# Performance work log

Hardware: AMD Instinct MI355X
Metric: run time of the kernel (lower is better)

Reference implementation:

```python
import jax, jax.numpy as jnp
import numpy as np

B, N, NODE_DIM = 64, 64, 192
H = 256          # node_hidden_dim
PDIM = 64        # property_embedding_dim
NUM_EDGE_TYPE = 5
T = 4            # message-passing rounds
E = 16384        # total edges (flattened batched graph)
E_SEL = 65536    # selected candidate pairs


def setup_inputs() -> dict:
    key = jax.random.key(0)
    ks = jax.random.split(key, 24)
    def g(k, shape, scale=0.05):
        return jax.random.normal(k, shape, dtype=jnp.float32) * scale
    inp = {
        "x": jax.random.normal(ks[0], (B, N, NODE_DIM), dtype=jnp.float32),
        "edge_index": jax.random.randint(ks[1], (2, E), 0, B * N, dtype=jnp.int32),
        "edge_attr": jax.random.uniform(ks[2], (E, NUM_EDGE_TYPE), dtype=jnp.float32),
        "props": jax.random.normal(ks[3], (B, 1), dtype=jnp.float32),
        "sel_b": jax.random.randint(ks[4], (E_SEL,), 0, B, dtype=jnp.int32),
        "sel_i": jax.random.randint(ks[5], (E_SEL,), 0, N, dtype=jnp.int32),
        "sel_j": jax.random.randint(ks[6], (E_SEL,), 0, N, dtype=jnp.int32),
        "golden_edge": jax.random.randint(ks[7], (E_SEL,), 0, NUM_EDGE_TYPE, dtype=jnp.int32),
        # parameters
        "W_prop": g(ks[8], (1, PDIM)), "b_prop": jnp.zeros((PDIM,), jnp.float32),
        "W_in": g(ks[9], (NODE_DIM, H)), "b_in": jnp.zeros((H,), jnp.float32),
        "W_msg": g(ks[10], (H + NUM_EDGE_TYPE, H)), "b_msg": jnp.zeros((H,), jnp.float32),
        "W_upd": g(ks[11], (2 * H, H)), "b_upd": jnp.zeros((H,), jnp.float32),
        "W_add": g(ks[12], (H + PDIM, H)), "b_add": jnp.zeros((H,), jnp.float32),
        "W1": g(ks[13], (2 * H, H)), "b1": jnp.zeros((H,), jnp.float32),
        "W2": g(ks[14], (H, H)), "b2": jnp.zeros((H,), jnp.float32),
        "W3": g(ks[15], (H, 2 * H)), "b3": jnp.zeros((2 * H,), jnp.float32),
        "W_out": g(ks[16], (2 * H, NUM_EDGE_TYPE)), "b_out": jnp.zeros((NUM_EDGE_TYPE,), jnp.float32),
    }
    return inp


def reference(x, edge_index, edge_attr, props, sel_b, sel_i, sel_j, golden_edge,
              W_prop, b_prop, W_in, b_in, W_msg, b_msg, W_upd, b_upd,
              W_add, b_add, W1, b1, W2, b2, W3, b3, W_out, b_out):
    BN = B * N
    node_x = x.reshape(BN, NODE_DIM)
    src, dst = edge_index[0], edge_index[1]

    # --- GNN node embedding (t rounds of message passing, opaque Encoder.embed_node) ---
    h = jax.nn.relu(node_x @ W_in + b_in)                       # [BN, H]
    for _ in range(T):
        msg_in = jnp.concatenate([h[src], edge_attr], axis=-1)  # [E, H+num_edge_type]
        msg = jax.nn.relu(msg_in @ W_msg + b_msg)               # [E, H]
        agg = jax.ops.segment_sum(msg, dst, num_segments=BN)    # [BN, H]
        h = jax.nn.relu(jnp.concatenate([h, agg], axis=-1) @ W_upd + b_upd)

    node_emb = h.reshape(B, N, H)

    # --- property conditioning + addition linear ---
    prop = props @ W_prop + b_prop                               # [B, PDIM]
    propp = jnp.broadcast_to(prop[:, None, :], (B, N, PDIM))
    node_embg = jnp.concatenate([node_emb, propp], axis=-1) @ W_add + b_add  # [B, N, H]

    # --- gather selected (src, dst) pairs directly (equiv. to repeat_interleave + boolean mask) ---
    flat = node_embg.reshape(BN, H)
    src_e = flat[sel_b * N + sel_i]                              # [E_SEL, H]
    dst_e = flat[sel_b * N + sel_j]                              # [E_SEL, H]
    pair = jnp.concatenate([src_e, dst_e], axis=-1)              # [E_SEL, 2H]

    # --- edge predictor MLP (3 layers, ReLU between) + output linear ---
    h1 = jax.nn.relu(pair @ W1 + b1)
    h2 = jax.nn.relu(h1 @ W2 + b2)
    h3 = h2 @ W3 + b3
    logits = h3 @ W_out + b_out                                  # [E_SEL, num_edge_type]

    # --- cross entropy (mean) ---
    logp = jax.nn.log_softmax(logits, axis=-1)
    loss = -jnp.mean(jnp.take_along_axis(logp, golden_edge[:, None].astype(jnp.int32), axis=-1))
    return loss
```

## Files before the change

kernel.cpp:

```cpp
#include <hip/hip_runtime.h>
#include <math.h>

#define BN 4096
#define N_PER_B 64
#define NE 16384
#define NSEL 65536
#define NET 5
#define PD 64
#define H1STR 260
#define FSTR 264

typedef float f32x4 __attribute__((ext_vector_type(4)));
typedef float f32x16 __attribute__((ext_vector_type(16)));
typedef short short8 __attribute__((ext_vector_type(8)));
typedef short short4v __attribute__((ext_vector_type(4)));

__device__ __forceinline__ unsigned short f2bf(float f) {
    unsigned int u = __builtin_bit_cast(unsigned int, f);
    u += 0x7fff + ((u >> 16) & 1);
    return (unsigned short)(u >> 16);
}
__device__ __forceinline__ float bf_lo(unsigned int u) {
    return __builtin_bit_cast(float, u << 16);
}
__device__ __forceinline__ float bf_hi(unsigned int u) {
    return __builtin_bit_cast(float, u & 0xffff0000u);
}
__device__ __forceinline__ unsigned int pack2(float a, float b) {
    return (unsigned)f2bf(a) | ((unsigned)f2bf(b) << 16);
}
__device__ __forceinline__ short8 ld_frag(const unsigned short* p) {
    const short4v lo = *(const short4v*)(p);
    const short4v hi = *(const short4v*)(p + 4);
    return __builtin_shufflevector(lo, hi, 0, 1, 2, 3, 4, 5, 6, 7);
}
__device__ __forceinline__ unsigned int addrelu2(unsigned int a, unsigned int b, unsigned int c) {
    const float lo = fmaxf(bf_lo(a) + bf_lo(b) + bf_lo(c), 0.f);
    const float hi = fmaxf(bf_hi(a) + bf_hi(b) + bf_hi(c), 0.f);
    return pack2(lo, hi);
}

__global__ __launch_bounds__(256) void k_hist(const int* __restrict__ eidx,
                                              int* __restrict__ deg)
{
    const int e = blockIdx.x * 256 + threadIdx.x;
    atomicAdd(&deg[eidx[NE + e]], 1);
}

__global__ __launch_bounds__(256) void csr_scan(const int* __restrict__ deg,
                                                int* __restrict__ row_start,
                                                int* __restrict__ cursor)
{
    __shared__ int sums[256];
    const int tid = threadIdx.x;
    const int base = tid * 16;
    int local[16];
    int s = 0;
    #pragma unroll
    for (int i = 0; i < 16; ++i) { local[i] = s; s += deg[base + i]; }
    sums[tid] = s;
    __syncthreads();
    for (int off = 1; off < 256; off <<= 1) {
        const int v = sums[tid];
        const int add = (tid >= off) ? sums[tid - off] : 0;
        __syncthreads();
        sums[tid] = v + add;
        __syncthreads();
    }
    const int offset = (tid == 0) ? 0 : sums[tid - 1];
    #pragma unroll
    for (int i = 0; i < 16; ++i) {
        const int v = offset + local[i];
        row_start[base + i] = v;
        cursor[base + i] = v;
    }
    if (tid == 255) row_start[4096] = NE;
}

__global__ __launch_bounds__(256) void csr_scatter(const int* __restrict__ eidx,
                                                   int* __restrict__ cursor,
                                                   int* __restrict__ srcs,
                                                   int* __restrict__ epos)
{
    const int e = blockIdx.x * 256 + threadIdx.x;
    const int pos = atomicAdd(&cursor[eidx[NE + e]], 1);
    srcs[pos] = eidx[e];
    epos[e] = pos;
}

__global__ __launch_bounds__(256) void k_pre(
    const float* __restrict__ W_in, const float* __restrict__ W_msg,
    const float* __restrict__ W_upd, const float* __restrict__ W_add,
    const float* __restrict__ W1, const float* __restrict__ W2,
    const float* __restrict__ W3, const float* __restrict__ b3,
    const float* __restrict__ W_out, const float* __restrict__ b_out,
    const float* __restrict__ props, const float* __restrict__ W_prop,
    const float* __restrict__ b_prop, const float* __restrict__ b_add,
    const float* __restrict__ b_msg, const float* __restrict__ eattr,
    const int* __restrict__ epos,
    unsigned short* __restrict__ wbf, unsigned short* __restrict__ WfT,
    float* __restrict__ bfv, float* __restrict__ prop_add,
    unsigned short* __restrict__ ETc)
{
    __shared__ __align__(16) char smem[16704];
    const int blk = blockIdx.x;
    const int tid = threadIdx.x;

    if (blk < 128) {
        float (*s)[65] = (float(*)[65])smem;
        const int wsel = blk >> 4;
        const int sub = blk & 15;
        const float* src; unsigned short* dst; int K = 256;
        switch (wsel) {
            case 0: src = W_in;              dst = wbf;                         K = 192; break;
            case 1: src = W_msg;             dst = wbf + 49152;                 break;
            case 2: src = W_upd;             dst = wbf + 49152 + 65536;         break;
            case 3: src = W_upd + 256 * 256; dst = wbf + 49152 + 2 * 65536;     break;
            case 4: src = W_add;             dst = wbf + 49152 + 3 * 65536;     break;
            case 5: src = W1;                dst = wbf + 49152 + 4 * 65536;     break;
            case 6: src = W1 + 256 * 256;    dst = wbf + 49152 + 5 * 65536;     break;
            default: src = W2;               dst = wbf + 49152 + 6 * 65536;     break;
        }
        const int k0 = (sub >> 2) * 64;
        const int n0 = (sub & 3) * 64;
        if (k0 >= K) return;
        const int tn = tid & 63;
        const int tg = tid >> 6;
        #pragma unroll
        for (int i = 0; i < 16; ++i) {
            const int kk = tg * 16 + i;
            s[kk][tn] = src[(size_t)(k0 + kk) * 256 + n0 + tn];
        }
        __syncthreads();
        #pragma unroll
        for (int i = 0; i < 16; ++i) {
            const int nn = tg * 16 + i;
            dst[(size_t)(n0 + nn) * K + k0 + tn] = f2bf(s[tn][nn]);
        }
    } else if (blk < 192) {
        const int b = blk - 128;
        const float pv = props[b];
        float acc = b_add[tid];
        for (int p = 0; p < PD; ++p) {
            const float e = fmaf(pv, W_prop[p], b_prop[p]);
            acc = fmaf(e, W_add[(256 + p) * 256 + tid], acc);
        }
        prop_add[b * 256 + tid] = acc;
    } else if (blk < 449) {
        float* part = (float*)smem;
        const int cb = blk - 192;
        float acc[NET] = {0.f, 0.f, 0.f, 0.f, 0.f};
        #pragma unroll
        for (int rep = 0; rep < 2; ++rep) {
            const int j = rep * 256 + tid;
            const float wv = (cb < 256) ? W3[(size_t)cb * 512 + j] : b3[j];
            #pragma unroll
            for (int t = 0; t < NET; ++t) acc[t] = fmaf(wv, W_out[j * NET + t], acc[t]);
        }
        #pragma unroll
        for (int t = 0; t < NET; ++t)
            for (int off = 32; off >= 1; off >>= 1) acc[t] += __shfl_down(acc[t], off);
        if ((tid & 63) == 0) {
            #pragma unroll
            for (int t = 0; t < NET; ++t) part[(tid >> 6) * NET + t] = acc[t];
        }
        __syncthreads();
        if (tid == 0) {
            float s[NET];
            #pragma unroll
            for (int t = 0; t < NET; ++t)
                s[t] = part[t] + part[NET + t] + part[2 * NET + t] + part[3 * NET + t];
            if (cb < 256) {
                #pragma unroll
                for (int t = 0; t < NET; ++t) WfT[t * 256 + cb] = f2bf(s[t]);
                #pragma unroll
                for (int t = NET; t < 16; ++t) WfT[t * 256 + cb] = 0;
            } else {
                #pragma unroll
                for (int t = 0; t < NET; ++t) bfv[t] = s[t] + b_out[t];
            }
        }
    } else {
        float* ea = (float*)smem;
        int* eposs = (int*)(smem + 2560 + 64);
        const int eb = (blk - 449) * 128;
        if (tid < 160)
            *(float4*)&ea[tid * 4] = *(const float4*)(eattr + (size_t)eb * 5 + tid * 4);
        if (tid < 128) eposs[tid] = epos[eb + tid];
        __syncthreads();
        const float* Wme = W_msg + 256 * 256;
        const float w0 = Wme[0 * 256 + tid];
        const float w1 = Wme[1 * 256 + tid];
        const float w2 = Wme[2 * 256 + tid];
        const float w3 = Wme[3 * 256 + tid];
        const float w4 = Wme[4 * 256 + tid];
        const float bm = b_msg[tid];
        for (int i = 0; i < 128; ++i) {
            const float* a = ea + i * 5;
            float v = bm;
            v = fmaf(a[0], w0, v); v = fmaf(a[1], w1, v); v = fmaf(a[2], w2, v);
            v = fmaf(a[3], w3, v); v = fmaf(a[4], w4, v);
            ETc[(size_t)eposs[i] * 256 + tid] = f2bf(v);
        }
    }
}

__global__ __launch_bounds__(1024) void fstep(
    const float* __restrict__ x, const unsigned short* __restrict__ hbuf,
    const unsigned short* __restrict__ Pin, const unsigned short* __restrict__ ETc,
    const int* __restrict__ row_start, const int* __restrict__ srcs,
    const unsigned short* __restrict__ WaT, const unsigned short* __restrict__ WbT,
    const float* __restrict__ bias1,
    const unsigned short* __restrict__ Wp2T, const float* __restrict__ prop_add,
    const unsigned short* __restrict__ W1aT, const unsigned short* __restrict__ W1bT,
    unsigned short* __restrict__ hout, unsigned short* __restrict__ out1,
    unsigned short* __restrict__ out2, int mode)
{
    __shared__ __align__(16) unsigned short Hg[16 * FSTR];
    __shared__ __align__(16) unsigned short Ag[16 * FSTR];
    __shared__ __align__(16) unsigned short Hs[16 * FSTR];
    __shared__ __align__(16) unsigned short H2s[16 * FSTR];
    const int tid = threadIdx.x;
    const int w = tid >> 6;
    const int lane = tid & 63;
    const int q = lane >> 4;
    const int tx = lane & 15;
    const int m0 = blockIdx.x * 16;
    const int col = w * 16 + tx;

    if (mode != 0) {
        {
            const int r = tid >> 6;
            const int c4 = (tid & 63) * 4;
            *(uint2*)&Hg[r * FSTR + c4] =
                *(const uint2*)(hbuf + (size_t)(m0 + r) * 256 + c4);
        }
        {
            const int node = m0 + w;
            const int beg = row_start[node];
            const int end = row_start[node + 1];
            const int c = lane * 4;
            float a0 = 0.f, a1 = 0.f, a2 = 0.f, a3 = 0.f;
            for (int idx = beg; idx < end; ++idx) {
                const int src = srcs[idx];
                const uint2 pu = *(const uint2*)(Pin + (size_t)src * 256 + c);
                const uint2 eu = *(const uint2*)(ETc + (size_t)idx * 256 + c);
                a0 += fmaxf(bf_lo(pu.x) + bf_lo(eu.x), 0.f);
                a1 += fmaxf(bf_hi(pu.x) + bf_hi(eu.x), 0.f);
                a2 += fmaxf(bf_lo(pu.y) + bf_lo(eu.y), 0.f);
                a3 += fmaxf(bf_hi(pu.y) + bf_hi(eu.y), 0.f);
            }
            uint2 o; o.x = pack2(a0, a1); o.y = pack2(a2, a3);
            *(uint2*)&Ag[w * FSTR + c] = o;
        }
        __syncthreads();
    }

    f32x4 acc = (f32x4)0.f;
    if (mode == 0) {
        #pragma unroll
        for (int s = 0; s < 6; ++s) {
            const int k0 = s * 32;
            const float* ap = x + (size_t)(m0 + tx) * 192 + k0 + q * 8;
            const float4 v0 = *(const float4*)ap;
            const float4 v1 = *(const float4*)(ap + 4);
            short8 af;
            af[0] = (short)f2bf(v0.x); af[1] = (short)f2bf(v0.y);
            af[2] = (short)f2bf(v0.z); af[3] = (short)f2bf(v0.w);
            af[4] = (short)f2bf(v1.x); af[5] = (short)f2bf(v1.y);
            af[6] = (short)f2bf(v1.z); af[7] = (short)f2bf(v1.w);
            const short8 bfr = *(const short8*)(WaT + (size_t)col * 192 + k0 + q * 8);
            acc = __builtin_amdgcn_mfma_f32_16x16x32_bf16(af, bfr, acc, 0, 0, 0);
        }
    } else {
        #pragma unroll
        for (int s = 0; s < 8; ++s) {
            const int k0 = s * 32;
            const short8 af = *(const short8*)&Hg[tx * FSTR + k0 + q * 8];
            const short8 bfr = *(const short8*)(WaT + (size_t)col * 256 + k0 + q * 8);
            acc = __builtin_amdgcn_mfma_f32_16x16x32_bf16(af, bfr, acc, 0, 0, 0);
        }
        #pragma unroll
        for (int s = 0; s < 8; ++s) {
            const int k0 = s * 32;
            const short8 af = *(const short8*)&Ag[tx * FSTR + k0 + q * 8];
            const short8 bfr = *(const short8*)(WbT + (size_t)col * 256 + k0 + q * 8);
            acc = __builtin_amdgcn_mfma_f32_16x16x32_bf16(af, bfr, acc, 0, 0, 0);
        }
    }
    {
        const float bv = bias1[col];
        #pragma unroll
        for (int r = 0; r < 4; ++r) {
            const int row = q * 4 + r;
            const unsigned short us = f2bf(fmaxf(acc[r] + bv, 0.f));
            Hs[row * FSTR + col] = us;
            if (mode < 2) hout[(size_t)(m0 + row) * 256 + col] = us;
        }
    }
    __syncthreads();

    acc = (f32x4)0.f;
    #pragma unroll
    for (int s = 0; s < 8; ++s) {
        const int k0 = s * 32;
        const short8 af = *(const short8*)&Hs[tx * FSTR + k0 + q * 8];
        const short8 bfr = *(const short8*)(Wp2T + (size_t)col * 256 + k0 + q * 8);
        acc = __builtin_amdgcn_mfma_f32_16x16x32_bf16(af, bfr, acc, 0, 0, 0);
    }
    if (mode < 2) {
        #pragma unroll
        for (int r = 0; r < 4; ++r)
            out1[(size_t)(m0 + q * 4 + r) * 256 + col] = f2bf(acc[r]);
        return;
    }
    {
        const float pv = prop_add[(m0 >> 6) * 256 + col];
        #pragma unroll
        for (int r = 0; r < 4; ++r)
            H2s[(q * 4 + r) * FSTR + col] = f2bf(acc[r] + pv);
    }
    __syncthreads();

    for (int which = 0; which < 2; ++which) {
        const unsigned short* WT = which ? W1bT : W1aT;
        unsigned short* op = which ? out2 : out1;
        acc = (f32x4)0.f;
        #pragma unroll
        for (int s = 0; s < 8; ++s) {
            const int k0 = s * 32;
            const short8 af = *(const short8*)&H2s[tx * FSTR + k0 + q * 8];
            const short8 bfr = *(const short8*)(WT + (size_t)col * 256 + k0 + q * 8);
            acc = __builtin_amdgcn_mfma_f32_16x16x32_bf16(af, bfr, acc, 0, 0, 0);
        }
        #pragma unroll
        for (int r = 0; r < 4; ++r)
            op[(size_t)(m0 + q * 4 + r) * 256 + col] = f2bf(acc[r]);
    }
}

__global__ __launch_bounds__(512) void pair_k(
    const unsigned short* __restrict__ A1t, const unsigned short* __restrict__ A2t,
    const float* __restrict__ b1, const unsigned short* __restrict__ W2T,
    const float* __restrict__ b2, const unsigned short* __restrict__ WfT,
    const float* __restrict__ bfv,
    const int* __restrict__ sel_b, const int* __restrict__ sel_i,
    const int* __restrict__ sel_j, const int* __restrict__ golden,
    float* __restrict__ out)
{
    __shared__ __align__(16) unsigned short sbuf[64 * H1STR];
    __shared__ __align__(16) unsigned short b1s[256];
    __shared__ float Lg[64 * 8];
    __shared__ int sidx[64], didx[64], gold[64];

    const int tid = threadIdx.x;
    const int w = tid >> 6;
    const int lane = tid & 63;
    const int q = lane >> 4;
    const int tx = lane & 15;
    const int m = lane & 31;
    const int hh = lane >> 5;
    const int e0 = blockIdx.x * 64;

    if (tid < 64) {
        const int e = e0 + tid;
        const int b = sel_b[e];
        sidx[tid] = b * N_PER_B + sel_i[e];
        didx[tid] = b * N_PER_B + sel_j[e];
        gold[tid] = golden[e];
    }
    if (tid < 256) b1s[tid] = f2bf(b1[tid]);
    __syncthreads();

    {
        const int p = tid >> 3;
        const int chn = tid & 7;
        const unsigned short* r1 = A1t + (size_t)sidx[p] * 256 + chn * 32;
        const unsigned short* r2 = A2t + (size_t)didx[p] * 256 + chn * 32;
        unsigned short* dbase = sbuf + p * H1STR + chn * 32;
        #pragma unroll
        for (int g = 0; g < 4; ++g) {
            const uint4 u1 = *(const uint4*)(r1 + g * 8);
            const uint4 u2 = *(const uint4*)(r2 + g * 8);
            const uint4 ub = *(const uint4*)(b1s + chn * 32 + g * 8);
            uint2 lo2, hi2;
            lo2.x = addrelu2(u1.x, u2.x, ub.x);
            lo2.y = addrelu2(u1.y, u2.y, ub.y);
            hi2.x = addrelu2(u1.z, u2.z, ub.z);
            hi2.y = addrelu2(u1.w, u2.w, ub.w);
            *(uint2*)(dbase + g * 8) = lo2;
            *(uint2*)(dbase + g * 8 + 4) = hi2;
        }
    }
    __syncthreads();

    const int pt = w & 1;
    const int cg = w >> 1;
    f32x16 acc[2];
    acc[0] = (f32x16)0.f; acc[1] = (f32x16)0.f;

    const unsigned short* arow = sbuf + (size_t)(pt * 32 + m) * H1STR + hh * 8;
    const unsigned short* bb0 = W2T + (size_t)(cg * 64 + m) * 256 + hh * 8;
    #pragma unroll 4
    for (int s = 0; s < 16; ++s) {
        const short8 af = ld_frag(arow + s * 16);
        #pragma unroll
        for (int cc = 0; cc < 2; ++cc) {
            const short8 bfr = *(const short8*)(bb0 + (size_t)cc * 32 * 256 + s * 16);
            acc[cc] = __builtin_amdgcn_mfma_f32_32x32x16_bf16(af, bfr, acc[cc], 0, 0, 0);
        }
    }
    __syncthreads();

    #pragma unroll
    for (int cc = 0; cc < 2; ++cc) {
        const int col = cg * 64 + cc * 32 + m;
        const float bv = b2[col];
        #pragma unroll
        for (int reg = 0; reg < 16; ++reg) {
            const int prow = pt * 32 + (reg & 3) + 8 * (reg >> 2) + 4 * hh;
            sbuf[prow * H1STR + col] = f2bf(fmaxf(acc[cc][reg] + bv, 0.f));
        }
    }
    __syncthreads();

    if (w < 4) {
        f32x4 accL = (f32x4)0.f;
        const unsigned short* a2row = sbuf + (size_t)(w * 16 + tx) * H1STR + q * 8;
        const unsigned short* bWf = WfT + (size_t)tx * 256 + q * 8;
        #pragma unroll
        for (int s = 0; s < 8; ++s) {
            const short8 af = ld_frag(a2row + s * 32);
            const short8 bfr = *(const short8*)(bWf + s * 32);
            accL = __builtin_amdgcn_mfma_f32_16x16x32_bf16(af, bfr, accL, 0, 0, 0);
        }
        if (tx < NET) {
            const float bb = bfv[tx];
            #pragma unroll
            for (int reg = 0; reg < 4; ++reg)
                Lg[(w * 16 + q * 4 + reg) * 8 + tx] = accL[reg] + bb;
        }
    }
    __syncthreads();

    if (tid < 64) {
        float lg[NET];
        #pragma unroll
        for (int t = 0; t < NET; ++t) lg[t] = Lg[tid * 8 + t];
        float mx = lg[0];
        #pragma unroll
        for (int t = 1; t < NET; ++t) mx = fmaxf(mx, lg[t]);
        float s = 0.f;
        #pragma unroll
        for (int t = 0; t < NET; ++t) s += expf(lg[t] - mx);
        float ls = mx + logf(s) - lg[gold[tid]];
        #pragma unroll
        for (int off = 32; off >= 1; off >>= 1) ls += __shfl_xor(ls, off);
        if (tid == 0) atomicAdd(out, ls * (1.0f / NSEL));
    }
}

extern "C" void kernel_launch(void* const* d_in, const int* in_sizes, int n_in,
                              void* d_out, int out_size, void* d_ws, size_t ws_size,
                              hipStream_t stream) {
    (void)in_sizes; (void)n_in; (void)out_size; (void)ws_size;
    const float* x      = (const float*)d_in[0];
    const int*   eidx   = (const int*)d_in[1];
    const float* eattr  = (const float*)d_in[2];
    const float* props  = (const float*)d_in[3];
    const int*   sel_b  = (const int*)d_in[4];
    const int*   sel_i  = (const int*)d_in[5];
    const int*   sel_j  = (const int*)d_in[6];
    const int*   golden = (const int*)d_in[7];
    const float* W_prop = (const float*)d_in[8];
    const float* b_prop = (const float*)d_in[9];
    const float* W_in   = (const float*)d_in[10];
    const float* b_in   = (const float*)d_in[11];
    const float* W_msg  = (const float*)d_in[12];
    const float* b_msg  = (const float*)d_in[13];
    const float* W_upd  = (const float*)d_in[14];
    const float* b_upd  = (const float*)d_in[15];
    const float* W_add  = (const float*)d_in[16];
    const float* b_add  = (const float*)d_in[17];
    const float* W1     = (const float*)d_in[18];
    const float* b1     = (const float*)d_in[19];
    const float* W2     = (const float*)d_in[20];
    const float* b2     = (const float*)d_in[21];
    const float* W3     = (const float*)d_in[22];
    const float* b3     = (const float*)d_in[23];
    const float* W_out  = (const float*)d_in[24];
    const float* b_out  = (const float*)d_in[25];

    const size_t SEG = (size_t)BN * 256;
    unsigned short* P0   = (unsigned short*)d_ws;
    unsigned short* P1   = P0 + SEG;
    unsigned short* hA   = P1 + SEG;
    unsigned short* hB   = hA + SEG;
    unsigned short* ETc  = hB + SEG;
    unsigned short* wbf  = ETc + (size_t)NE * 256;
    unsigned short* W_inT  = wbf;
    unsigned short* WmT    = wbf + 49152;
    unsigned short* WuaT   = WmT + 65536;
    unsigned short* WubT   = WuaT + 65536;
    unsigned short* W_addT = WubT + 65536;
    unsigned short* W1aT   = W_addT + 65536;
    unsigned short* W1bT   = W1aT + 65536;
    unsigned short* W2T    = W1bT + 65536;
    unsigned short* WfT    = W2T + 65536;
    float* prop_add = (float*)(WfT + 4096);
    float* bfv = prop_add + 64 * 256;
    int* deg       = (int*)(bfv + 16);
    int* row_start = deg + 4096;
    int* cursor    = row_start + 4104;
    int* srcs      = cursor + 4096;
    int* epos      = srcs + NE;

    hipMemsetAsync(deg, 0, 4096 * sizeof(int), stream);
    k_hist<<<NE / 256, 256, 0, stream>>>(eidx, deg);
    csr_scan<<<1, 256, 0, stream>>>(deg, row_start, cursor);
    csr_scatter<<<NE / 256, 256, 0, stream>>>(eidx, cursor, srcs, epos);
    k_pre<<<577, 256, 0, stream>>>(W_in, W_msg, W_upd, W_add, W1, W2, W3, b3,
                                   W_out, b_out, props, W_prop, b_prop, b_add,
                                   b_msg, eattr, epos, wbf, WfT, bfv, prop_add, ETc);

    fstep<<<256, 1024, 0, stream>>>(x, nullptr, nullptr, ETc, row_start, srcs,
                                    W_inT, nullptr, b_in, WmT, nullptr, nullptr, nullptr,
                                    hA, P0, nullptr, 0);
    fstep<<<256, 1024, 0, stream>>>(nullptr, hA, P0, ETc, row_start, srcs,
                                    WuaT, WubT, b_upd, WmT, nullptr, nullptr, nullptr,
                                    hB, P1, nullptr, 1);
    fstep<<<256, 1024, 0, stream>>>(nullptr, hB, P1, ETc, row_start, srcs,
                                    WuaT, WubT, b_upd, WmT, nullptr, nullptr, nullptr,
                                    hA, P0, nullptr, 1);
    fstep<<<256, 1024, 0, stream>>>(nullptr, hA, P0, ETc, row_start, srcs,
                                    WuaT, WubT, b_upd, WmT, nullptr, nullptr, nullptr,
                                    hB, P1, nullptr, 1);
    fstep<<<256, 1024, 0, stream>>>(nullptr, hB, P1, ETc, row_start, srcs,
                                    WuaT, WubT, b_upd, W_addT, prop_add, W1aT, W1bT,
                                    nullptr, P0, hA, 2);

    hipMemsetAsync(d_out, 0, sizeof(float), stream);
    pair_k<<<NSEL / 64, 512, 0, stream>>>(P0, hA, b1, W2T, b2, WfT, bfv,
                                          sel_b, sel_i, sel_j, golden, (float*)d_out);
}
```

Measured before the change: 275.2 us.

## Process four pair tiles per block with W2 fragments held in registers

Result: faster. 252.1 us (-8.4%).

```diff
diff --git a/kernel.cpp b/kernel.cpp
--- a/kernel.cpp
+++ b/kernel.cpp
@@ -9,6 +9,7 @@
 #define PD 64
 #define H1STR 260
 #define FSTR 264
+#define PTILES 4
 
 typedef float f32x4 __attribute__((ext_vector_type(4)));
 typedef float f32x16 __attribute__((ext_vector_type(16)));
@@ -339,7 +340,7 @@
     }
 }
 
-__global__ __launch_bounds__(512) void pair_k(
+__global__ __launch_bounds__(512, 1) void pair_k(
     const unsigned short* __restrict__ A1t, const unsigned short* __restrict__ A2t,
     const float* __restrict__ b1, const unsigned short* __restrict__ W2T,
     const float* __restrict__ b2, const unsigned short* __restrict__ WfT,
@@ -351,7 +352,7 @@
     __shared__ __align__(16) unsigned short sbuf[64 * H1STR];
     __shared__ __align__(16) unsigned short b1s[256];
     __shared__ float Lg[64 * 8];
-    __shared__ int sidx[64], didx[64], gold[64];
+    __shared__ int sidx[64 * PTILES], didx[64 * PTILES], gold[64 * PTILES];
 
     const int tid = threadIdx.x;
     const int w = tid >> 6;
@@ -360,9 +361,9 @@
     const int tx = lane & 15;
     const int m = lane & 31;
     const int hh = lane >> 5;
-    const int e0 = blockIdx.x * 64;
-
-    if (tid < 64) {
+    const int e0 = blockIdx.x * 64 * PTILES;
+
+    if (tid < 64 * PTILES) {
         const int e = e0 + tid;
         const int b = sel_b[e];
         sidx[tid] = b * N_PER_B + sel_i[e];
@@ -370,94 +371,109 @@
         gold[tid] = golden[e];
     }
     if (tid < 256) b1s[tid] = f2bf(b1[tid]);
-    __syncthreads();
-
-    {
-        const int p = tid >> 3;
-        const int chn = tid & 7;
-        const unsigned short* r1 = A1t + (size_t)sidx[p] * 256 + chn * 32;
-        const unsigned short* r2 = A2t + (size_t)didx[p] * 256 + chn * 32;
-        unsigned short* dbase = sbuf + p * H1STR + chn * 32;
-        #pragma unroll
-        for (int g = 0; g < 4; ++g) {
-            const uint4 u1 = *(const uint4*)(r1 + g * 8);
-            const uint4 u2 = *(const uint4*)(r2 + g * 8);
-            const uint4 ub = *(const uint4*)(b1s + chn * 32 + g * 8);
-            uint2 lo2, hi2;
-            lo2.x = addrelu2(u1.x, u2.x, ub.x);
-            lo2.y = addrelu2(u1.y, u2.y, ub.y);
-            hi2.x = addrelu2(u1.z, u2.z, ub.z);
-            hi2.y = addrelu2(u1.w, u2.w, ub.w);
-            *(uint2*)(dbase + g * 8) = lo2;
-            *(uint2*)(dbase + g * 8 + 4) = hi2;
-        }
-    }
-    __syncthreads();
 
     const int pt = w & 1;
     const int cg = w >> 1;
-    f32x16 acc[2];
-    acc[0] = (f32x16)0.f; acc[1] = (f32x16)0.f;
-
-    const unsigned short* arow = sbuf + (size_t)(pt * 32 + m) * H1STR + hh * 8;
-    const unsigned short* bb0 = W2T + (size_t)(cg * 64 + m) * 256 + hh * 8;
-    #pragma unroll 4
-    for (int s = 0; s < 16; ++s) {
-        const short8 af = ld_frag(arow + s * 16);
+    short8 Breg[32];
+    {
+        const unsigned short* bb = W2T + (size_t)(cg * 64 + m) * 256 + hh * 8;
+        #pragma unroll
+        for (int cc = 0; cc < 2; ++cc)
+            #pragma unroll
+            for (int s = 0; s < 16; ++s)
+                Breg[cc * 16 + s] = *(const short8*)(bb + (size_t)cc * 32 * 256 + s * 16);
+    }
+    __syncthreads();
+
+    float total = 0.f;
+
+    for (int t = 0; t < PTILES; ++t) {
+        {
+            const int hw = tid >> 5;
+            #pragma unroll
+            for (int j = 0; j < 4; ++j) {
+                const int p = j * 16 + hw;
+                const unsigned short* r1 = A1t + (size_t)sidx[t * 64 + p] * 256 + m * 8;
+                const unsigned short* r2 = A2t + (size_t)didx[t * 64 + p] * 256 + m * 8;
+                const uint4 u1 = *(const uint4*)r1;
+                const uint4 u2 = *(const uint4*)r2;
+                const uint4 ub = *(const uint4*)(b1s + m * 8);
+                uint2 lo2, hi2;
+                lo2.x = addrelu2(u1.x, u2.x, ub.x);
+                lo2.y = addrelu2(u1.y, u2.y, ub.y);
+                hi2.x = addrelu2(u1.z, u2.z, ub.z);
+                hi2.y = addrelu2(u1.w, u2.w, ub.w);
+                unsigned short* dbase = sbuf + p * H1STR + m * 8;
+                *(uint2*)(dbase) = lo2;
+                *(uint2*)(dbase + 4) = hi2;
+            }
+        }
+        __syncthreads();
+
+        f32x16 acc0 = (f32x16)0.f;
+        f32x16 acc1 = (f32x16)0.f;
+        {
+            const unsigned short* arow = sbuf + (size_t)(pt * 32 + m) * H1STR + hh * 8;
+            #pragma unroll
+            for (int s = 0; s < 16; ++s) {
+                const short8 af = ld_frag(arow + s * 16);
+                acc0 = __builtin_amdgcn_mfma_f32_32x32x16_bf16(af, Breg[s], acc0, 0, 0, 0);
+                acc1 = __builtin_amdgcn_mfma_f32_32x32x16_bf16(af, Breg[16 + s], acc1, 0, 0, 0);
+            }
+        }
+        __syncthreads();
+
         #pragma unroll
         for (int cc = 0; cc < 2; ++cc) {
-            const short8 bfr = *(const short8*)(bb0 + (size_t)cc * 32 * 256 + s * 16);
-            acc[cc] = __builtin_amdgcn_mfma_f32_32x32x16_bf16(af, bfr, acc[cc], 0, 0, 0);
-        }
-    }
-    __syncthreads();
-
-    #pragma unroll
-    for (int cc = 0; cc < 2; ++cc) {
-        const int col = cg * 64 + cc * 32 + m;
-        const float bv = b2[col];
-        #pragma unroll
-        for (int reg = 0; reg < 16; ++reg) {
-            const int prow = pt * 32 + (reg & 3) + 8 * (reg >> 2) + 4 * hh;
-            sbuf[prow * H1STR + col] = f2bf(fmaxf(acc[cc][reg] + bv, 0.f));
-        }
-    }
-    __syncthreads();
-
-    if (w < 4) {
-        f32x4 accL = (f32x4)0.f;
-        const unsigned short* a2row = sbuf + (size_t)(w * 16 + tx) * H1STR + q * 8;
-        const unsigned short* bWf = WfT + (size_t)tx * 256 + q * 8;
-        #pragma unroll
-        for (int s = 0; s < 8; ++s) {
-            const short8 af = ld_frag(a2row + s * 32);
-            const short8 bfr = *(const short8*)(bWf + s * 32);
-            accL = __builtin_amdgcn_mfma_f32_16x16x32_bf16(af, bfr, accL, 0, 0, 0);
-        }
-        if (tx < NET) {
-            const float bb = bfv[tx];
-            #pragma unroll
-            for (int reg = 0; reg < 4; ++reg)
-                Lg[(w * 16 + q * 4 + reg) * 8 + tx] = accL[reg] + bb;
-        }
-    }
-    __syncthreads();
-
-    if (tid < 64) {
-        float lg[NET];
-        #pragma unroll
-        for (int t = 0; t < NET; ++t) lg[t] = Lg[tid * 8 + t];
-        float mx = lg[0];
-        #pragma unroll
-        for (int t = 1; t < NET; ++t) mx = fmaxf(mx, lg[t]);
-        float s = 0.f;
-        #pragma unroll
-        for (int t = 0; t < NET; ++t) s += expf(lg[t] - mx);
-        float ls = mx + logf(s) - lg[gold[tid]];
-        #pragma unroll
-        for (int off = 32; off >= 1; off >>= 1) ls += __shfl_xor(ls, off);
-        if (tid == 0) atomicAdd(out, ls * (1.0f / NSEL));
-    }
+            const f32x16* ap = cc ? &acc1 : &acc0;
+            const int col = cg * 64 + cc * 32 + m;
+            const float bv = b2[col];
+            #pragma unroll
+            for (int reg = 0; reg < 16; ++reg) {
+                const int prow = pt * 32 + (reg & 3) + 8 * (reg >> 2) + 4 * hh;
+                sbuf[prow * H1STR + col] = f2bf(fmaxf((*ap)[reg] + bv, 0.f));
+            }
+        }
+        __syncthreads();
+
+        if (w < 4) {
+            f32x4 accL = (f32x4)0.f;
+            const unsigned short* a2row = sbuf + (size_t)(w * 16 + tx) * H1STR + q * 8;
+            const unsigned short* bWf = WfT + (size_t)tx * 256 + q * 8;
+            #pragma unroll
+            for (int s = 0; s < 8; ++s) {
+                const short8 af = ld_frag(a2row + s * 32);
+                const short8 bfr = *(const short8*)(bWf + s * 32);
+                accL = __builtin_amdgcn_mfma_f32_16x16x32_bf16(af, bfr, accL, 0, 0, 0);
+            }
+            if (tx < NET) {
+                const float bb = bfv[tx];
+                #pragma unroll
+                for (int reg = 0; reg < 4; ++reg)
+                    Lg[(w * 16 + q * 4 + reg) * 8 + tx] = accL[reg] + bb;
+            }
+        }
+        __syncthreads();
+
+        if (tid < 64) {
+            float lg[NET];
+            #pragma unroll
+            for (int tt = 0; tt < NET; ++tt) lg[tt] = Lg[tid * 8 + tt];
+            float mx = lg[0];
+            #pragma unroll
+            for (int tt = 1; tt < NET; ++tt) mx = fmaxf(mx, lg[tt]);
+            float s = 0.f;
+            #pragma unroll
+            for (int tt = 0; tt < NET; ++tt) s += expf(lg[tt] - mx);
+            float ls = mx + logf(s) - lg[gold[t * 64 + tid]];
+            #pragma unroll
+            for (int off = 32; off >= 1; off >>= 1) ls += __shfl_xor(ls, off);
+            total += ls;
+        }
+        __syncthreads();
+    }
+
+    if (tid == 0) atomicAdd(out, total * (1.0f / NSEL));
 }
 
 extern "C" void kernel_launch(void* const* d_in, const int* in_sizes, int n_in,
@@ -540,6 +556,6 @@
                                     nullptr, P0, hA, 2);
 
     hipMemsetAsync(d_out, 0, sizeof(float), stream);
-    pair_k<<<NSEL / 64, 512, 0, stream>>>(P0, hA, b1, W2T, b2, WfT, bfv,
-                                          sel_b, sel_i, sel_j, golden, (float*)d_out);
-}
+    pair_k<<<256, 512, 0, stream>>>(P0, hA, b1, W2T, b2, WfT, bfv,
+                                    sel_b, sel_i, sel_j, golden, (float*)d_out);
+}
```
